# Performance work log

Measured on AMD Instinct MI355X. Metric: run time of the kernel, lower is better.

Reference implementation:

```python
import jax, jax.numpy as jnp
import numpy as np
import math

B, S, H = 2, 2048, 3072
N_HEADS, N_KV_HEADS, HEAD_DIM = 32, 8, 96
ROPE_THETA = 10000.0
OP_SIZE = N_HEADS * HEAD_DIM + 2 * N_KV_HEADS * HEAD_DIM  # 4608


def setup_inputs() -> dict:
    key = jax.random.key(0)
    k1, k2, k3 = jax.random.split(key, 3)
    hidden_states = jax.random.normal(k1, (B, S, H), dtype=jnp.float32)
    # additive causal mask: 0 on/below diagonal, -inf-ish above
    neg = jnp.finfo(jnp.float32).min
    causal = jnp.where(jnp.tril(jnp.ones((S, S), dtype=bool)), 0.0, neg)
    attention_mask = jnp.broadcast_to(causal[None, None], (B, 1, S, S)).astype(jnp.float32)
    # torch nn.Linear convention: weight [out_features, in_features]
    w_qkv = jax.random.normal(k2, (OP_SIZE, H), dtype=jnp.float32) * 0.02
    w_o = jax.random.normal(k3, (H, H), dtype=jnp.float32) * 0.02
    position_ids = jnp.broadcast_to(jnp.arange(S, dtype=jnp.int32)[None], (B, S))
    return {"hidden_states": hidden_states, "attention_mask": attention_mask,
            "w_qkv": w_qkv, "w_o": w_o, "position_ids": position_ids}


def _rotate_half(x):
    half = x.shape[-1] // 2
    return jnp.concatenate([-x[..., half:], x[..., :half]], axis=-1)


def _rope_cos_sin(position_ids, head_dim, theta):
    # Phi3RotaryEmbedding (no scaling)
    inv_freq = 1.0 / (theta ** (jnp.arange(0, head_dim, 2, dtype=jnp.float32) / head_dim))
    freqs = position_ids.astype(jnp.float32)[:, :, None] * inv_freq[None, None, :]  # [b,s,d/2]
    emb = jnp.concatenate([freqs, freqs], axis=-1)  # [b,s,d]
    return jnp.cos(emb), jnp.sin(emb)


def reference(hidden_states, attention_mask, w_qkv, w_o, position_ids):
    b, s, _ = hidden_states.shape
    qkv = jnp.einsum('bsh,oh->bso', hidden_states, w_qkv)  # quantized qkv_proj (fp emulation)
    q_pos = N_HEADS * HEAD_DIM
    kv_pos = q_pos + N_KV_HEADS * HEAD_DIM
    q = qkv[..., :q_pos].reshape(b, s, N_HEADS, HEAD_DIM).transpose(0, 2, 1, 3)
    k = qkv[..., q_pos:kv_pos].reshape(b, s, N_KV_HEADS, HEAD_DIM).transpose(0, 2, 1, 3)
    v = qkv[..., kv_pos:].reshape(b, s, N_KV_HEADS, HEAD_DIM).transpose(0, 2, 1, 3)

    cos, sin = _rope_cos_sin(position_ids, HEAD_DIM, ROPE_THETA)
    cos, sin = cos[:, None], sin[:, None]  # [b,1,s,d]
    q = q * cos + _rotate_half(q) * sin
    k = k * cos + _rotate_half(k) * sin

    # repeat_kv: GQA expand kv heads to query heads
    groups = N_HEADS // N_KV_HEADS
    k = jnp.repeat(k, groups, axis=1)  # [b,h,s,d]
    v = jnp.repeat(v, groups, axis=1)

    # quantized QK^T matmul (fp emulation)
    scores = jnp.einsum('bhqd,bhkd->bhqk', q, k) / math.sqrt(HEAD_DIM)
    scores = scores + attention_mask  # additive causal mask
    attn = jax.nn.softmax(scores.astype(jnp.float32), axis=-1).astype(v.dtype)
    # dropout p=0 (eval); quantized attn @ V matmul (fp emulation)
    out = jnp.einsum('bhqk,bhkd->bhqd', attn, v)
    out = out.transpose(0, 2, 1, 3).reshape(b, s, N_HEADS * HEAD_DIM)
    out = jnp.einsum('bso,ho->bsh', out, w_o)  # quantized o_proj
    return out
```

## Files before the change

kernel.cpp:

```cpp
#include <hip/hip_runtime.h>
#include <hip/hip_bf16.h>
#include <math.h>

#define S_LEN 2048
#define HDIM  3072
#define NH    32
#define NKV   8
#define HD    96
#define OPSZ  4608
#define QPOS  3072
#define KPOS  3840

typedef short  short8 __attribute__((ext_vector_type(8)));
typedef short  short4v __attribute__((ext_vector_type(4)));
typedef float  f32x4  __attribute__((ext_vector_type(4)));
typedef unsigned short us4 __attribute__((ext_vector_type(4)));

typedef __attribute__((address_space(1))) const unsigned int* gas1_t;
typedef __attribute__((address_space(3))) unsigned int* las3_t;

__device__ __forceinline__ void gl_lds16(const void* g, void* l) {
  __builtin_amdgcn_global_load_lds((gas1_t)g, (las3_t)l, 16, 0, 0);
}

#define VMCNT(n) asm volatile("s_waitcnt vmcnt(" #n ")" ::: "memory")

__device__ __forceinline__ unsigned short f2b(float f) {
  union { float f; unsigned u; } x; x.f = f;
  unsigned r = x.u + 0x7fffu + ((x.u >> 16) & 1u);
  return (unsigned short)(r >> 16);
}
__device__ __forceinline__ float b2f(unsigned short b) {
  union { unsigned u; float f; } x; x.u = ((unsigned)b) << 16;
  return x.f;
}

__device__ __forceinline__ short4v pack_bf16_4(float p0, float p1, float p2, float p3) {
  unsigned u0 = __builtin_bit_cast(unsigned, p0) + 0x8000u;
  unsigned u1 = __builtin_bit_cast(unsigned, p1) + 0x8000u;
  unsigned u2 = __builtin_bit_cast(unsigned, p2) + 0x8000u;
  unsigned u3 = __builtin_bit_cast(unsigned, p3) + 0x8000u;
  unsigned lo = __builtin_amdgcn_perm(u1, u0, 0x07060302u);
  unsigned hi = __builtin_amdgcn_perm(u3, u2, 0x07060302u);
  uint2 q; q.x = lo; q.y = hi;
  return __builtin_bit_cast(short4v, q);
}

__global__ __launch_bounds__(256) void k_convert3(const float* __restrict__ s0, int n0,
                                                  const float* __restrict__ s1, int n1,
                                                  const float* __restrict__ s2, int n2,
                                                  unsigned short* __restrict__ dst) {
  int i = blockIdx.x * 256 + threadIdx.x;
  const float* src; int local;
  if (i < n0)            { src = s0; local = i; }
  else if (i < n0 + n1)  { src = s1; local = i - n0; }
  else if (i < n0 + n1 + n2) { src = s2; local = i - n0 - n1; }
  else return;
  float4 v = ((const float4*)src)[local];
  us4 o;
  o[0] = f2b(v.x); o[1] = f2b(v.y); o[2] = f2b(v.z); o[3] = f2b(v.w);
  ((us4*)dst)[i] = o;
}

template<int OUTBF, int NF>
__global__ __launch_bounds__(512, 2) void k_gemm_pipe(const unsigned short* __restrict__ A,
                                                      const unsigned short* __restrict__ Bt,
                                                      void* __restrict__ Cout,
                                                      int M, int N, int K, int GX) {
  constexpr int BN    = NF * 32;
  constexpr int GSLOT = 8192 + BN * 32;
  __shared__ unsigned short lds[4 * GSLOT];

  const int NC = K >> 5;
  const int tid = threadIdx.x;
  const int lane = tid & 63;
  const int wave = tid >> 6;
  const int wm = wave & 3, wn = wave >> 2;
  const int lr = lane & 15, lg = lane >> 4;
  const int prh = lr >> 1, bit = lr & 1;

  const int nwg = gridDim.x;
  const int id  = blockIdx.x;
  const int sw  = (id & 7) * (nwg >> 3) + (id >> 3);
  const int bx  = sw % GX, by = sw / GX;
  const int m0 = by * 256, n0 = bx * BN;

  const int i0 = tid, i1 = 512 + tid;
  const int p0 = i0 >> 3, g0 = (i0 & 7) ^ (p0 & 7);
  const int p1 = i1 >> 3, g1 = (i1 & 7) ^ (p1 & 7);
  const unsigned short* aG0 = A + (size_t)(m0 + 2 * p0 + (g0 >> 2)) * K + (g0 & 3) * 8;
  const unsigned short* aG1 = A + (size_t)(m0 + 2 * p1 + (g1 >> 2)) * K + (g1 & 3) * 8;
  const int aO0 = i0 * 8, aO1 = i1 * 8;

  const int q0 = i0 >> 3, h0 = (i0 & 7) ^ (q0 & 7);
  const int q1 = i1 >> 3, h1 = (i1 & 7) ^ (q1 & 7);
  const unsigned short* bG0 = Bt + (size_t)(n0 + 2 * q0 + (h0 >> 2)) * K + (h0 & 3) * 8;
  const unsigned short* bG1 = Bt + (size_t)(n0 + 2 * q1 + (h1 >> 2)) * K + (h1 & 3) * 8;
  const int bO0 = 8192 + i0 * 8, bO1 = 8192 + i1 * 8;
  const int i2 = 1024 + (tid & 127);
  const int q2 = i2 >> 3, h2 = (i2 & 7) ^ (q2 & 7);
  const unsigned short* bG2 = Bt + (size_t)(n0 + 2 * q2 + (h2 >> 2)) * K + (h2 & 3) * 8;
  const int bO2 = 8192 + i2 * 8;
  const bool xb = (NF == 9) ? (tid < 128) : (tid < 256);

  auto stageA = [&](int c) {
    unsigned short* sb = &lds[(c & 3) * GSLOT];
    gl_lds16(aG0 + c * 32, sb + aO0);
    gl_lds16(aG1 + c * 32, sb + aO1);
  };
  auto stageB = [&](int c) {
    unsigned short* sb = &lds[(c & 3) * GSLOT];
    gl_lds16(bG0 + c * 32, sb + bO0);
    if constexpr (NF == 9) {
      gl_lds16(bG1 + c * 32, sb + bO1);
      if (xb) gl_lds16(bG2 + c * 32, sb + bO2);
    } else {
      if (xb) gl_lds16(bG1 + c * 32, sb + bO1);
    }
  };

  const int gp  = ((bit << 2) + lg) ^ prh;
  const int aRd = wm * 2048 + prh * 64 + gp * 8;
  const int bRd = 8192 + wn * (BN * 16) + prh * 64 + gp * 8;

  f32x4 acc[4][NF];
#pragma unroll
  for (int mf = 0; mf < 4; mf++)
#pragma unroll
    for (int nf = 0; nf < NF; nf++)
#pragma unroll
      for (int r = 0; r < 4; r++) acc[mf][nf][r] = 0.0f;

#define VM_STEADY() do { \
    if constexpr (NF == 9) { if (wave < 2) { VMCNT(10); } else { VMCNT(8); } } \
    else                   { if (wave < 4) { VMCNT(8);  } else { VMCNT(6); } } } while (0)
#define VM_TAIL1() do { \
    if constexpr (NF == 9) { if (wave < 2) { VMCNT(5); } else { VMCNT(4); } } \
    else                   { if (wave < 4) { VMCNT(4); } else { VMCNT(3); } } } while (0)

  stageA(0); stageB(0);
  stageA(1); stageB(1);
  stageA(2); stageB(2);
  VM_STEADY();
  __builtin_amdgcn_s_barrier();
  __builtin_amdgcn_sched_barrier(0);

  for (int c = 0; c < NC; ++c) {
    const unsigned short* sb = &lds[(c & 3) * GSLOT];
    short8 af[4], bf[NF];
#pragma unroll
    for (int mf = 0; mf < 4; mf++) af[mf] = *(const short8*)&sb[aRd + mf * 512];
#pragma unroll
    for (int nf = 0; nf < NF; nf++) bf[nf] = *(const short8*)&sb[bRd + nf * 512];
    if (c + 3 < NC) { stageA(c + 3); stageB(c + 3); }
    __builtin_amdgcn_s_setprio(1);
#pragma unroll
    for (int nf = 0; nf < NF; nf++)
#pragma unroll
      for (int mf = 0; mf < 4; mf++)
        acc[mf][nf] = __builtin_amdgcn_mfma_f32_16x16x32_bf16(af[mf], bf[nf], acc[mf][nf], 0, 0, 0);
    __builtin_amdgcn_s_setprio(0);
    if (c < NC - 3)       { VM_STEADY(); }
    else if (c == NC - 3) { VM_TAIL1(); }
    else if (c == NC - 2) { VMCNT(0); }
    if (c + 1 < NC) {
      __builtin_amdgcn_sched_barrier(0);
      __builtin_amdgcn_s_barrier();
      __builtin_amdgcn_sched_barrier(0);
    }
  }

#pragma unroll
  for (int mf = 0; mf < 4; mf++)
#pragma unroll
    for (int nf = 0; nf < NF; nf++)
#pragma unroll
      for (int r = 0; r < 4; r++) {
        int row = m0 + wm * 64 + mf * 16 + lg * 4 + r;
        int col = n0 + wn * (BN / 2) + nf * 16 + lr;
        if (OUTBF) ((unsigned short*)Cout)[(size_t)row * N + col] = f2b(acc[mf][nf][r]);
        else       ((float*)Cout)[(size_t)row * N + col] = acc[mf][nf][r];
      }
#undef VM_STEADY
#undef VM_TAIL1
}

__global__ __launch_bounds__(256) void k_rope(const unsigned short* __restrict__ qkv,
                                              const int* __restrict__ pos_ids,
                                              unsigned short* __restrict__ Qb,
                                              unsigned short* __restrict__ Kb) {
  __shared__ float cs[96], sn[96];
  int blk = blockIdx.x;
  int b = blk >> 11, s = blk & 2047;
  int t = threadIdx.x;
  int pos = pos_ids[blk];
  if (t < 48) {
    float e = -((float)(2 * t) / 96.0f) * 9.210340371976184f;
    float invf = __expf(e);
    float a = (float)pos * invf;
    float c, si;
    __sincosf(a, &si, &c);
    cs[t] = c; cs[t + 48] = c;
    sn[t] = si; sn[t + 48] = si;
  }
  __syncthreads();
  const unsigned short* row = qkv + (size_t)blk * OPSZ;
  const float qscale = 0.1020620726159658f;
  for (int o = t; o < KPOS; o += 256) {
    int d = o % 96;
    float x  = b2f(row[o]);
    float xp = b2f(row[d < 48 ? o + 48 : o - 48]);
    float rot = (d < 48) ? -xp : xp;
    float val = x * cs[d] + rot * sn[d];
    if (o < QPOS) {
      int h = o / 96;
      Qb[((size_t)(b * NH + h) * S_LEN + s) * HD + d] = f2b(val * qscale);
    } else {
      int kh = (o - QPOS) / 96;
      Kb[((size_t)(b * NKV + kh) * S_LEN + s) * HD + d] = f2b(val);
    }
  }
}

__global__ __launch_bounds__(256) void k_vtrans(const unsigned short* __restrict__ qkv,
                                                unsigned short* __restrict__ Vt) {
  int blk = blockIdx.x;
  int st = blk & 31, kh = (blk >> 5) & 7, b = blk >> 8;
  int s0 = st * 64;
  __shared__ unsigned short tile[96][65];
  int t = threadIdx.x;
#pragma unroll
  for (int c = 0; c < 24; c++) {
    int idx = c * 256 + t;
    int ls = idx / 96, d = idx % 96;
    tile[d][ls] = qkv[(size_t)(b * S_LEN + s0 + ls) * OPSZ + KPOS + kh * 96 + d];
  }
  __syncthreads();
#pragma unroll
  for (int c = 0; c < 24; c++) {
    int idx = c * 256 + t;
    int d = idx >> 6, ls = idx & 63;
    Vt[((size_t)(b * NKV + kh) * HD + d) * S_LEN + s0 + ls] = tile[d][ls];
  }
}

__global__ __launch_bounds__(512, 4) void k_flash(const unsigned short* __restrict__ Qb,
                                                  const unsigned short* __restrict__ Kb,
                                                  const unsigned short* __restrict__ Vt,
                                                  unsigned short* __restrict__ attn) {
  __shared__ unsigned short smem[24832];
  __shared__ float Lsh[128 * 8];
  unsigned short* Ks  = smem;
  unsigned short* Vs  = smem + 6144;
  unsigned short* QPs = smem + 12288;
  float* Osh = (float*)smem;

  int blk = blockIdx.x;
  int j = blk & 7;
  int h = (blk >> 3) & 31;
  int b = blk >> 8;
  int kh = h >> 2;
  int tid = threadIdx.x, lane = tid & 63, wave = tid >> 6;
  int lr = lane & 15, lg = lane >> 4;
  int qg = wave >> 1, kg = wave & 1;
  const int swz = (lr >> 1) & 3;

  const unsigned short* ksrc = Kb + (size_t)(b * NKV + kh) * S_LEN * HD;
  const unsigned short* vsrc = Vt + (size_t)(b * NKV + kh) * HD * S_LEN;

  for (int half = 0; half < 2; half++) {
    int qtile = half ? (15 - j) : j;
    int q0 = qtile * 128;
    const unsigned short* qsrc = Qb + ((size_t)(b * NH + h) * S_LEN + q0) * HD;

    __syncthreads();
#pragma unroll
    for (int p = 0; p < 3; p++) {
      int gi = p * 512 + tid;
      int pl = gi >> 9, wp = gi & 511;
      int r = wp >> 2, s = wp & 3;
      int l = pl * 4 + (s ^ ((r >> 1) & 3));
      gl_lds16(qsrc + (size_t)r * HD + l * 8, &QPs[gi * 8]);
    }
#pragma unroll
    for (int p = 0; p < 3; p++) {
      int gi = p * 512 + tid;
      if (gi < 768) {
        int pl = gi >> 8, wp = gi & 255;
        int r = wp >> 2, s = wp & 3;
        int l = pl * 4 + (s ^ ((r >> 1) & 3));
        gl_lds16(ksrc + (size_t)r * HD + l * 8, &Ks[gi * 8]);
      } else {
        int gi2 = gi - 768;
        int pl = (gi2 >= 384) ? 1 : 0;
        int rem = gi2 - pl * 384;
        int d = rem >> 2, s = rem & 3;
        int l = s ^ ((d >> 1) & 3);
        gl_lds16(vsrc + (size_t)d * S_LEN + pl * 32 + l * 8, &Vs[gi2 * 8]);
      }
    }
    __syncthreads();

    short8 qf[2][3];
#pragma unroll
    for (int qt = 0; qt < 2; qt++)
#pragma unroll
      for (int ds = 0; ds < 3; ds++)
        qf[qt][ds] = *(const short8*)&QPs[ds * 4096 + (qg * 32 + qt * 16 + lr) * 32 + (lg ^ swz) * 8];

    f32x4 oacc[2][6];
#pragma unroll
    for (int qt = 0; qt < 2; qt++)
#pragma unroll
      for (int dt = 0; dt < 6; dt++)
#pragma unroll
        for (int r = 0; r < 4; r++) oacc[qt][dt][r] = 0.0f;
    float lsum[2] = {0.0f, 0.0f};

    int nk = qtile * 2 + 2;
    for (int it = 0; it < nk; it++) {
      int k0 = it * 64;
      f32x4 sc[2][2];
#pragma unroll
      for (int kt = 0; kt < 2; kt++)
#pragma unroll
        for (int qt = 0; qt < 2; qt++)
#pragma unroll
          for (int r = 0; r < 4; r++) sc[kt][qt][r] = 0.0f;
#pragma unroll
      for (int kt = 0; kt < 2; kt++)
#pragma unroll
        for (int ds = 0; ds < 3; ds++) {
          short8 kf = *(const short8*)&Ks[ds * 2048 + (kg * 32 + kt * 16 + lr) * 32 + (lg ^ swz) * 8];
#pragma unroll
          for (int qt = 0; qt < 2; qt++)
            sc[kt][qt] = __builtin_amdgcn_mfma_f32_16x16x32_bf16(kf, qf[qt][ds], sc[kt][qt], 0, 0, 0);
        }
      if (it >= nk - 2) {
#pragma unroll
        for (int kt = 0; kt < 2; kt++)
#pragma unroll
          for (int qt = 0; qt < 2; qt++) {
            int qrow = q0 + qg * 32 + qt * 16 + lr;
            int keyb = k0 + kg * 32 + kt * 16 + lg * 4;
#pragma unroll
            for (int r = 0; r < 4; r++)
              if (keyb + r > qrow) sc[kt][qt][r] = -3.0e38f;
          }
      }
      short4v pf[2][2];
#pragma unroll
      for (int kt = 0; kt < 2; kt++)
#pragma unroll
        for (int qt = 0; qt < 2; qt++) {
          float p0 = __expf(sc[kt][qt][0]);
          float p1 = __expf(sc[kt][qt][1]);
          float p2 = __expf(sc[kt][qt][2]);
          float p3 = __expf(sc[kt][qt][3]);
          lsum[qt] += (p0 + p1) + (p2 + p3);
          pf[kt][qt] = pack_bf16_4(p0, p1, p2, p3);
        }
#pragma unroll
      for (int kt = 0; kt < 2; kt++)
#pragma unroll
        for (int dt = 0; dt < 6; dt++) {
          short4v vf = *(const short4v*)&Vs[kg * 3072 + (dt * 16 + lr) * 32 +
                                           (((kt * 2 + (lg >> 1)) ^ swz) * 8) + (lg & 1) * 4];
#pragma unroll
          for (int qt = 0; qt < 2; qt++)
            oacc[qt][dt] = __builtin_amdgcn_mfma_f32_16x16x16bf16_1k(pf[kt][qt], vf, oacc[qt][dt], 0, 0, 0);
        }
      __syncthreads();
      if (it + 1 < nk) {
        int k0n = (it + 1) * 64;
#pragma unroll
        for (int p = 0; p < 3; p++) {
          int gi = p * 512 + tid;
          if (gi < 768) {
            int pl = gi >> 8, wp = gi & 255;
            int r = wp >> 2, s = wp & 3;
            int l = pl * 4 + (s ^ ((r >> 1) & 3));
            gl_lds16(ksrc + (size_t)(k0n + r) * HD + l * 8, &Ks[gi * 8]);
          } else {
            int gi2 = gi - 768;
            int pl = (gi2 >= 384) ? 1 : 0;
            int rem = gi2 - pl * 384;
            int d = rem >> 2, s = rem & 3;
            int l = s ^ ((d >> 1) & 3);
            gl_lds16(vsrc + (size_t)d * S_LEN + k0n + pl * 32 + l * 8, &Vs[gi2 * 8]);
          }
        }
        __syncthreads();
      }
    }
    if (kg == 0) {
#pragma unroll
      for (int qt = 0; qt < 2; qt++)
#pragma unroll
        for (int dt = 0; dt < 6; dt++)
#pragma unroll
          for (int r = 0; r < 4; r++)
            Osh[(qg * 32 + qt * 16 + lg * 4 + r) * 97 + dt * 16 + lr] = oacc[qt][dt][r];
    }
#pragma unroll
    for (int qt = 0; qt < 2; qt++)
      Lsh[(qg * 32 + qt * 16 + lr) * 8 + kg * 4 + lg] = lsum[qt];
    __syncthreads();
    if (kg == 1) {
      float linv[2][4];
#pragma unroll
      for (int qt = 0; qt < 2; qt++)
#pragma unroll
        for (int r = 0; r < 4; r++) {
          int row = qg * 32 + qt * 16 + lg * 4 + r;
          float4 a = *(const float4*)&Lsh[row * 8];
          float4 c = *(const float4*)&Lsh[row * 8 + 4];
          linv[qt][r] = 1.0f / ((a.x + a.y + a.z + a.w) + (c.x + c.y + c.z + c.w));
        }
#pragma unroll
      for (int qt = 0; qt < 2; qt++)
#pragma unroll
        for (int dt = 0; dt < 6; dt++)
#pragma unroll
          for (int r = 0; r < 4; r++) {
            int rowl = qg * 32 + qt * 16 + lg * 4 + r;
            float v = Osh[rowl * 97 + dt * 16 + lr] + oacc[qt][dt][r];
            int row = q0 + rowl;
            int col = h * 96 + dt * 16 + lr;
            attn[(size_t)(b * S_LEN + row) * HDIM + col] = f2b(v * linv[qt][r]);
          }
    }
  }
}

extern "C" void kernel_launch(void* const* d_in, const int* in_sizes, int n_in,
                              void* d_out, int out_size, void* d_ws, size_t ws_size,
                              hipStream_t stream) {
  const float* hidden = (const float*)d_in[0];
  const float* w_qkv  = (const float*)d_in[2];
  const float* w_o    = (const float*)d_in[3];
  const int*   posids = (const int*)d_in[4];

  const size_t M = 4096;
  unsigned short* hidden_bf = (unsigned short*)d_ws;
  unsigned short* wqkv_bf   = hidden_bf + M * HDIM;
  unsigned short* wo_bf     = wqkv_bf + (size_t)OPSZ * HDIM;
  unsigned short* qkv_bf    = wo_bf + (size_t)HDIM * HDIM;
  unsigned short* Qb   = hidden_bf;
  unsigned short* Kb   = wqkv_bf;
  unsigned short* Vt   = wqkv_bf + (size_t)NKV * 2 * S_LEN * HD;
  unsigned short* attn = qkv_bf;

  int n4h = (int)(M * HDIM / 4);
  int n4q = (int)((size_t)OPSZ * HDIM / 4);
  int n4o = (int)((size_t)HDIM * HDIM / 4);
  int n4t = n4h + n4q + n4o;
  k_convert3<<<(n4t + 255) / 256, 256, 0, stream>>>(hidden, n4h, w_qkv, n4q, w_o, n4o,
                                                    hidden_bf);

  k_gemm_pipe<1, 9><<<256, 512, 0, stream>>>(hidden_bf, wqkv_bf, qkv_bf,
                                             (int)M, OPSZ, HDIM, OPSZ / 288);
  k_rope<<<(int)M, 256, 0, stream>>>(qkv_bf, posids, Qb, Kb);
  k_vtrans<<<2 * NKV * (S_LEN / 64), 256, 0, stream>>>(qkv_bf, Vt);
  k_flash<<<2 * NH * 8, 512, 0, stream>>>(Qb, Kb, Vt, attn);
  k_gemm_pipe<0, 6><<<256, 512, 0, stream>>>(attn, wo_bf, d_out,
                                             (int)M, HDIM, HDIM, HDIM / 192);
}
```

Measured before the change: 474.8 us.

## Double-buffer K/V tiles in flash attention to overlap loads with MFMA

Splits shared memory into two K/V slots and prefetches the next key tile with async global-to-LDS loads while the current tile is computed. Two barriers per iteration become one, with explicit vmcnt waits. This is meant to hide global load latency behind the QK and PV MFMAs. LDS use per block grows by about 24 KB, which may lower occupancy at 512 threads.

```diff
diff --git a/kernel.cpp b/kernel.cpp
--- a/kernel.cpp
+++ b/kernel.cpp
@@ -248,11 +248,9 @@
                                                   const unsigned short* __restrict__ Kb,
                                                   const unsigned short* __restrict__ Vt,
                                                   unsigned short* __restrict__ attn) {
-  __shared__ unsigned short smem[24832];
+  __shared__ unsigned short smem[36864];
   __shared__ float Lsh[128 * 8];
-  unsigned short* Ks  = smem;
-  unsigned short* Vs  = smem + 6144;
-  unsigned short* QPs = smem + 12288;
+  unsigned short* QPs = smem + 24576;
   float* Osh = (float*)smem;
 
   int blk = blockIdx.x;
@@ -268,10 +266,34 @@
   const unsigned short* ksrc = Kb + (size_t)(b * NKV + kh) * S_LEN * HD;
   const unsigned short* vsrc = Vt + (size_t)(b * NKV + kh) * HD * S_LEN;
 
+  auto stageKV = [&](int it, int sl) {
+    int k0 = it * 64;
+    unsigned short* Ksl = smem + sl * 6144;
+    unsigned short* Vsl = smem + 12288 + sl * 6144;
+#pragma unroll
+    for (int p = 0; p < 3; p++) {
+      int gi = p * 512 + tid;
+      if (gi < 768) {
+        int pl = gi >> 8, wp = gi & 255;
+        int r = wp >> 2, s = wp & 3;
+        int l = pl * 4 + (s ^ ((r >> 1) & 3));
+        gl_lds16(ksrc + (size_t)(k0 + r) * HD + l * 8, &Ksl[gi * 8]);
+      } else {
+        int gi2 = gi - 768;
+        int pl = (gi2 >= 384) ? 1 : 0;
+        int rem = gi2 - pl * 384;
+        int d = rem >> 2, s = rem & 3;
+        int l = s ^ ((d >> 1) & 3);
+        gl_lds16(vsrc + (size_t)d * S_LEN + k0 + pl * 32 + l * 8, &Vsl[gi2 * 8]);
+      }
+    }
+  };
+
   for (int half = 0; half < 2; half++) {
     int qtile = half ? (15 - j) : j;
     int q0 = qtile * 128;
     const unsigned short* qsrc = Qb + ((size_t)(b * NH + h) * S_LEN + q0) * HD;
+    int nk = qtile * 2 + 2;
 
     __syncthreads();
 #pragma unroll
@@ -282,24 +304,11 @@
       int l = pl * 4 + (s ^ ((r >> 1) & 3));
       gl_lds16(qsrc + (size_t)r * HD + l * 8, &QPs[gi * 8]);
     }
-#pragma unroll
-    for (int p = 0; p < 3; p++) {
-      int gi = p * 512 + tid;
-      if (gi < 768) {
-        int pl = gi >> 8, wp = gi & 255;
-        int r = wp >> 2, s = wp & 3;
-        int l = pl * 4 + (s ^ ((r >> 1) & 3));
-        gl_lds16(ksrc + (size_t)r * HD + l * 8, &Ks[gi * 8]);
-      } else {
-        int gi2 = gi - 768;
-        int pl = (gi2 >= 384) ? 1 : 0;
-        int rem = gi2 - pl * 384;
-        int d = rem >> 2, s = rem & 3;
-        int l = s ^ ((d >> 1) & 3);
-        gl_lds16(vsrc + (size_t)d * S_LEN + pl * 32 + l * 8, &Vs[gi2 * 8]);
-      }
-    }
-    __syncthreads();
+    stageKV(0, 0);
+    stageKV(1, 1);
+    VMCNT(3);
+    __builtin_amdgcn_s_barrier();
+    __builtin_amdgcn_sched_barrier(0);
 
     short8 qf[2][3];
 #pragma unroll
@@ -317,8 +326,11 @@
         for (int r = 0; r < 4; r++) oacc[qt][dt][r] = 0.0f;
     float lsum[2] = {0.0f, 0.0f};
 
-    int nk = qtile * 2 + 2;
     for (int it = 0; it < nk; it++) {
+      int sl = it & 1;
+      const unsigned short* Ksl = smem + sl * 6144;
+      const unsigned short* Vsl = smem + 12288 + sl * 6144;
+      if (it >= 1 && it + 1 < nk) stageKV(it + 1, (it + 1) & 1);
       int k0 = it * 64;
       f32x4 sc[2][2];
 #pragma unroll
@@ -331,7 +343,7 @@
       for (int kt = 0; kt < 2; kt++)
 #pragma unroll
         for (int ds = 0; ds < 3; ds++) {
-          short8 kf = *(const short8*)&Ks[ds * 2048 + (kg * 32 + kt * 16 + lr) * 32 + (lg ^ swz) * 8];
+          short8 kf = *(const short8*)&Ksl[ds * 2048 + (kg * 32 + kt * 16 + lr) * 32 + (lg ^ swz) * 8];
 #pragma unroll
           for (int qt = 0; qt < 2; qt++)
             sc[kt][qt] = __builtin_amdgcn_mfma_f32_16x16x32_bf16(kf, qf[qt][ds], sc[kt][qt], 0, 0, 0);
@@ -364,34 +376,16 @@
       for (int kt = 0; kt < 2; kt++)
 #pragma unroll
         for (int dt = 0; dt < 6; dt++) {
-          short4v vf = *(const short4v*)&Vs[kg * 3072 + (dt * 16 + lr) * 32 +
-                                           (((kt * 2 + (lg >> 1)) ^ swz) * 8) + (lg & 1) * 4];
+          short4v vf = *(const short4v*)&Vsl[kg * 3072 + (dt * 16 + lr) * 32 +
+                                            (((kt * 2 + (lg >> 1)) ^ swz) * 8) + (lg & 1) * 4];
 #pragma unroll
           for (int qt = 0; qt < 2; qt++)
             oacc[qt][dt] = __builtin_amdgcn_mfma_f32_16x16x16bf16_1k(pf[kt][qt], vf, oacc[qt][dt], 0, 0, 0);
         }
-      __syncthreads();
-      if (it + 1 < nk) {
-        int k0n = (it + 1) * 64;
-#pragma unroll
-        for (int p = 0; p < 3; p++) {
-          int gi = p * 512 + tid;
-          if (gi < 768) {
-            int pl = gi >> 8, wp = gi & 255;
-            int r = wp >> 2, s = wp & 3;
-            int l = pl * 4 + (s ^ ((r >> 1) & 3));
-            gl_lds16(ksrc + (size_t)(k0n + r) * HD + l * 8, &Ks[gi * 8]);
-          } else {
-            int gi2 = gi - 768;
-            int pl = (gi2 >= 384) ? 1 : 0;
-            int rem = gi2 - pl * 384;
-            int d = rem >> 2, s = rem & 3;
-            int l = s ^ ((d >> 1) & 3);
-            gl_lds16(vsrc + (size_t)d * S_LEN + k0n + pl * 32 + l * 8, &Vs[gi2 * 8]);
-          }
-        }
-        __syncthreads();
-      }
+      VMCNT(0);
+      __builtin_amdgcn_sched_barrier(0);
+      __builtin_amdgcn_s_barrier();
+      __builtin_amdgcn_sched_barrier(0);
     }
     if (kg == 0) {
 #pragma unroll
```

Result: no change. 482.3 us (+1.6%).
